# Kernel optimization log

Measured on AMD Instinct MI355X. Metric: run time of the kernel, lower is better.

Reference implementation:

```python
import jax, jax.numpy as jnp
import numpy as np

BN_EPS = 1e-5

def setup_inputs() -> dict:
    key = jax.random.key(0)
    ks = jax.random.split(key, 10)
    N, D, E, EL, L = 100000, 128, 1600000, 500000, 3
    return {
        "x": jax.random.normal(ks[0], (N, D), jnp.float32),
        "lin_w": jax.random.normal(ks[1], (D, D), jnp.float32) * 0.05,
        "lin_b": jax.random.normal(ks[2], (D,), jnp.float32) * 0.05,
        "W1": jax.random.normal(ks[3], (L, D, D), jnp.float32) * 0.05,
        "b1": jax.random.normal(ks[4], (L, D), jnp.float32) * 0.05,
        "gamma": jnp.ones((L, D), jnp.float32),
        "beta": jnp.zeros((L, D), jnp.float32),
        "W2": jax.random.normal(ks[5], (L, D, D), jnp.float32) * 0.05,
        "b2": jax.random.normal(ks[6], (L, D), jnp.float32) * 0.05,
        "edge_index": jax.random.randint(ks[7], (2, E), 0, N, jnp.int64),
        "edge_label_index": jax.random.randint(ks[8], (2, EL), 0, N, jnp.int64),
    }

def reference(x, lin_w, lin_b, W1, b1, gamma, beta, W2, b2, edge_index, edge_label_index):
    N = x.shape[0]
    src, dst = edge_index[0], edge_index[1]
    # node_lin: Linear(num_features -> hidden)
    h = x @ lin_w + lin_b  # [N, D]
    # 3 GINConv layers: out_i = MLP((1+eps)*h_i + sum_{j->i} h_j), eps = 0
    for l in range(3):
        agg = jax.ops.segment_sum(h[src], dst, num_segments=N)  # scatter-add over edges
        z = h + agg
        z = z @ W1[l] + b1[l]
        # BatchNorm1d in training mode: batch (per-node-dim) statistics, biased var
        mu = jnp.mean(z, axis=0)
        var = jnp.var(z, axis=0)
        z = (z - mu) * jax.lax.rsqrt(var + BN_EPS) * gamma[l] + beta[l]
        z = jax.nn.relu(z)
        z = z @ W2[l] + b2[l]
        h = jax.nn.relu(z)
    # Classifier: dot product of endpoint embeddings
    pred = jnp.sum(h[edge_label_index[0]] * h[edge_label_index[1]], axis=-1)  # [E_label]
    return pred
```

## Files before the change

kernel.cpp:

```cpp
#include <hip/hip_runtime.h>
#include <hip/hip_bf16.h>


typedef __attribute__((ext_vector_type(8))) short short8v;
typedef __attribute__((ext_vector_type(4))) float float4v;

#define NBLK_SORT 512

__device__ __forceinline__ unsigned short f2bf(float f) {
    union { float f; unsigned u; } v; v.f = f;
    unsigned u = v.u;
    unsigned r = u + 0x7fffu + ((u >> 16) & 1u);
    return (unsigned short)(r >> 16);
}
__device__ __forceinline__ float bf2f(unsigned short h) {
    union { unsigned u; float f; } v; v.u = ((unsigned)h) << 16;
    return v.f;
}
__device__ __forceinline__ float bfu_lo(unsigned u) {
    union { unsigned v; float f; } x; x.v = u << 16; return x.f;
}
__device__ __forceinline__ float bfu_hi(unsigned u) {
    union { unsigned v; float f; } x; x.v = u & 0xffff0000u; return x.f;
}
__device__ __forceinline__ unsigned pkbf(float x, float y) {
    __hip_bfloat162 t = __float22bfloat162_rn(float2{x, y});
    union { __hip_bfloat162 b; unsigned u; } c; c.b = t;
    return c.u;
}

__global__ __launch_bounds__(256) void prep_w(
    const float* __restrict__ lin_w, const float* __restrict__ W1,
    const float* __restrict__ W2,
    unsigned short* __restrict__ wt_hi, unsigned short* __restrict__ wt_lo)
{
    int idx = blockIdx.x * 256 + threadIdx.x;
    if (idx >= 7 * 16384) return;
    int m = idx >> 14;
    int r = idx & 16383;
    int k = r >> 7, n = r & 127;
    const float* src = (m == 0) ? lin_w
                     : (m <= 3) ? W1 + (size_t)(m - 1) * 16384
                                : W2 + (size_t)(m - 4) * 16384;
    float w = src[r];
    unsigned short hi = f2bf(w);
    unsigned short lo = f2bf(w - bf2f(hi));
    wt_hi[(size_t)m * 16384 + n * 128 + k] = hi;
    wt_lo[(size_t)m * 16384 + n * 128 + k] = lo;
}

__global__ __launch_bounds__(256) void chunk_count(
    const int* __restrict__ dst, int* __restrict__ cnt, int E, int nbc)
{
    __shared__ int l[1024];
    const int tid = threadIdx.x, b = blockIdx.x;
    for (int i = tid; i < nbc; i += 256) l[i] = 0;
    __syncthreads();
    const int per = (E + gridDim.x - 1) / gridDim.x;
    const int e0 = b * per, e1 = min(E, e0 + per);
    for (int e = e0 + tid; e < e1; e += 256)
        atomicAdd(&l[dst[e] >> 10], 1);
    __syncthreads();
    for (int c = tid; c < nbc; c += 256) cnt[c * gridDim.x + b] = l[c];
}

__global__ __launch_bounds__(256) void chunk_scan(
    int* __restrict__ cnt, int* __restrict__ chunkBase, int nbc)
{
    __shared__ int ctot[1024];
    __shared__ int cbase[1025];
    const int t = threadIdx.x;
    for (int c = t; c < nbc; c += 256) {
        int base = 0;
        for (int b = 0; b < NBLK_SORT; b++) {
            int x = cnt[c * NBLK_SORT + b];
            cnt[c * NBLK_SORT + b] = base;
            base += x;
        }
        ctot[c] = base;
    }
    __syncthreads();
    if (t == 0) {
        int acc = 0;
        for (int c = 0; c < nbc; c++) { cbase[c] = acc; acc += ctot[c]; }
        cbase[nbc] = acc;
    }
    __syncthreads();
    for (int c = t; c < nbc; c += 256) {
        const int cb = cbase[c];
        for (int b = 0; b < NBLK_SORT; b++) cnt[c * NBLK_SORT + b] += cb;
        chunkBase[c] = cb;
    }
    if (t == 0) chunkBase[nbc] = cbase[nbc];
}

__global__ __launch_bounds__(256) void bucket_scatter(
    const int* __restrict__ src, const int* __restrict__ dst,
    const int* __restrict__ cnt, int* __restrict__ temp, int E, int nbc)
{
    __shared__ int lcur[1024];
    const int tid = threadIdx.x, b = blockIdx.x;
    for (int c = tid; c < nbc; c += 256) lcur[c] = cnt[c * gridDim.x + b];
    __syncthreads();
    const int per = (E + gridDim.x - 1) / gridDim.x;
    const int e0 = b * per, e1 = min(E, e0 + per);
    for (int e = e0 + tid; e < e1; e += 256) {
        const int d = dst[e];
        const int pos = atomicAdd(&lcur[d >> 10], 1);
        temp[pos] = ((d & 1023) << 22) | src[e];
    }
}

__global__ __launch_bounds__(256) void chunk_place(
    const int* __restrict__ temp, const int* __restrict__ chunkBase,
    int* __restrict__ col, int* __restrict__ deg, int* __restrict__ rowptr,
    int N)
{
    __shared__ int lcnt[1024];
    __shared__ int lcur[1024];
    __shared__ int sh[256];
    const int tid = threadIdx.x, c = blockIdx.x;
    const int s = chunkBase[c], e2 = chunkBase[c + 1];

    for (int i = tid; i < 1024; i += 256) lcnt[i] = 0;
    __syncthreads();
    for (int i = s + tid; i < e2; i += 256)
        atomicAdd(&lcnt[((unsigned)temp[i]) >> 22], 1);
    __syncthreads();

    const int b4 = tid * 4;
    const int v0 = lcnt[b4], v1 = lcnt[b4 + 1], v2 = lcnt[b4 + 2], v3 = lcnt[b4 + 3];
    const int ts = v0 + v1 + v2 + v3;
    sh[tid] = ts;
    __syncthreads();
    for (int off = 1; off < 256; off <<= 1) {
        int x = (tid >= off) ? sh[tid - off] : 0;
        __syncthreads();
        sh[tid] += x;
        __syncthreads();
    }
    const int run = sh[tid] - ts;
    lcur[b4]     = s + run;
    lcur[b4 + 1] = s + run + v0;
    lcur[b4 + 2] = s + run + v0 + v1;
    lcur[b4 + 3] = s + run + v0 + v1 + v2;
    const int node0 = c << 10;
    if (node0 + b4 < N)     { deg[node0 + b4]     = v0; rowptr[node0 + b4]     = lcur[b4]; }
    if (node0 + b4 + 1 < N) { deg[node0 + b4 + 1] = v1; rowptr[node0 + b4 + 1] = lcur[b4 + 1]; }
    if (node0 + b4 + 2 < N) { deg[node0 + b4 + 2] = v2; rowptr[node0 + b4 + 2] = lcur[b4 + 2]; }
    if (node0 + b4 + 3 < N) { deg[node0 + b4 + 3] = v3; rowptr[node0 + b4 + 3] = lcur[b4 + 3]; }
    __syncthreads();

    for (int i = s + tid; i < e2; i += 256) {
        const unsigned p = (unsigned)temp[i];
        const int pos = atomicAdd(&lcur[p >> 22], 1);
        col[pos] = (int)(p & 0x3FFFFFu);
    }
}

__global__ __launch_bounds__(256) void gemm_mfma(
    const float* __restrict__ Ain32, const unsigned short* __restrict__ AinB,
    const int* __restrict__ rowptr, const int* __restrict__ deg,
    const int* __restrict__ col,
    const unsigned short* __restrict__ Wh, const unsigned short* __restrict__ Wl,
    const float* __restrict__ bias, const float* __restrict__ ss,
    unsigned short* __restrict__ outb, float* __restrict__ part,
    int N, int flags)
{
    __shared__ __align__(16) unsigned short As[64][136];
    const int tid = threadIdx.x;
    const int row0 = blockIdx.x * 64;

    if (flags & 32) {
        const int g = tid >> 4;
        const int l = tid & 15;
        #pragma unroll
        for (int rr = 0; rr < 4; rr++) {
            const int r = g + rr * 16;
            const int row = row0 + r;
            float4 a0 = make_float4(0.f, 0.f, 0.f, 0.f);
            float4 a1 = make_float4(0.f, 0.f, 0.f, 0.f);
            if (row < N) {
                const uint4 su = *(const uint4*)(AinB + (size_t)row * 128 + l * 8);
                a0.x = bfu_lo(su.x); a0.y = bfu_hi(su.x);
                a0.z = bfu_lo(su.y); a0.w = bfu_hi(su.y);
                a1.x = bfu_lo(su.z); a1.y = bfu_hi(su.z);
                a1.z = bfu_lo(su.w); a1.w = bfu_hi(su.w);
                const int start = rowptr[row];
                const int cnt = deg[row];
                int j = 0;
                for (; j + 1 < cnt; j += 2) {
                    const int c0i = col[start + j];
                    const int c1i = col[start + j + 1];
                    const uint4 u0 = *(const uint4*)(AinB + (size_t)c0i * 128 + l * 8);
                    const uint4 u1 = *(const uint4*)(AinB + (size_t)c1i * 128 + l * 8);
                    a0.x += bfu_lo(u0.x); a0.y += bfu_hi(u0.x);
                    a0.z += bfu_lo(u0.y); a0.w += bfu_hi(u0.y);
                    a1.x += bfu_lo(u0.z); a1.y += bfu_hi(u0.z);
                    a1.z += bfu_lo(u0.w); a1.w += bfu_hi(u0.w);
                    a0.x += bfu_lo(u1.x); a0.y += bfu_hi(u1.x);
                    a0.z += bfu_lo(u1.y); a0.w += bfu_hi(u1.y);
                    a1.x += bfu_lo(u1.z); a1.y += bfu_hi(u1.z);
                    a1.z += bfu_lo(u1.w); a1.w += bfu_hi(u1.w);
                }
                if (j < cnt) {
                    const int c0i = col[start + j];
                    const uint4 u0 = *(const uint4*)(AinB + (size_t)c0i * 128 + l * 8);
                    a0.x += bfu_lo(u0.x); a0.y += bfu_hi(u0.x);
                    a0.z += bfu_lo(u0.y); a0.w += bfu_hi(u0.y);
                    a1.x += bfu_lo(u0.z); a1.y += bfu_hi(u0.z);
                    a1.z += bfu_lo(u0.w); a1.w += bfu_hi(u0.w);
                }
            }
            uint4 uh;
            uh.x = pkbf(a0.x, a0.y);
            uh.y = pkbf(a0.z, a0.w);
            uh.z = pkbf(a1.x, a1.y);
            uh.w = pkbf(a1.z, a1.w);
            *(uint4*)&As[r][l * 8] = uh;
        }
    } else if (flags & 64) {
        for (int i = tid; i < 64 * 16; i += 256) {
            const int r = i >> 4, c8 = i & 15;
            const int row = row0 + r;
            if (row < N) {
                uint4 u = *(const uint4*)(AinB + (size_t)row * 128 + c8 * 8);
                if (flags & 1) {
                    float4 v0, v1;
                    v0.x = bfu_lo(u.x); v0.y = bfu_hi(u.x);
                    v0.z = bfu_lo(u.y); v0.w = bfu_hi(u.y);
                    v1.x = bfu_lo(u.z); v1.y = bfu_hi(u.z);
                    v1.z = bfu_lo(u.w); v1.w = bfu_hi(u.w);
                    const float4 sc0 = ((const float4*)ss)[c8 * 2];
                    const float4 sc1 = ((const float4*)ss)[c8 * 2 + 1];
                    const float4 sh0 = ((const float4*)(ss + 128))[c8 * 2];
                    const float4 sh1 = ((const float4*)(ss + 128))[c8 * 2 + 1];
                    v0.x = fmaxf(v0.x * sc0.x + sh0.x, 0.f);
                    v0.y = fmaxf(v0.y * sc0.y + sh0.y, 0.f);
                    v0.z = fmaxf(v0.z * sc0.z + sh0.z, 0.f);
                    v0.w = fmaxf(v0.w * sc0.w + sh0.w, 0.f);
                    v1.x = fmaxf(v1.x * sc1.x + sh1.x, 0.f);
                    v1.y = fmaxf(v1.y * sc1.y + sh1.y, 0.f);
                    v1.z = fmaxf(v1.z * sc1.z + sh1.z, 0.f);
                    v1.w = fmaxf(v1.w * sc1.w + sh1.w, 0.f);
                    u.x = pkbf(v0.x, v0.y);
                    u.y = pkbf(v0.z, v0.w);
                    u.z = pkbf(v1.x, v1.y);
                    u.w = pkbf(v1.z, v1.w);
                }
                *(uint4*)&As[r][c8 * 8] = u;
            } else {
                *(uint4*)&As[r][c8 * 8] = make_uint4(0, 0, 0, 0);
            }
        }
    } else {
        for (int i = tid; i < 64 * 32; i += 256) {
            const int r = i >> 5, c4 = i & 31;
            const int row = row0 + r;
            float4 v = make_float4(0.f, 0.f, 0.f, 0.f);
            if (row < N) v = ((const float4*)(Ain32 + (size_t)row * 128))[c4];
            uint2 uh;
            uh.x = pkbf(v.x, v.y);
            uh.y = pkbf(v.z, v.w);
            *(uint2*)&As[r][c4 * 4] = uh;
        }
    }
    __syncthreads();

    const int w    = tid >> 6;
    const int lane = tid & 63;
    const int ln   = lane & 15;
    const int lq   = lane >> 4;
    const int c0   = w * 32;

    float4v acc[4][2];
    #pragma unroll
    for (int nt = 0; nt < 2; nt++) {
        const float bv = bias[c0 + nt * 16 + ln];
        #pragma unroll
        for (int mt = 0; mt < 4; mt++) acc[mt][nt] = (float4v){bv, bv, bv, bv};
    }

    #pragma unroll
    for (int kc = 0; kc < 4; kc++) {
        const size_t b0 = (size_t)(c0 + ln) * 128 + kc * 32 + lq * 8;
        const size_t b1 = (size_t)(c0 + 16 + ln) * 128 + kc * 32 + lq * 8;
        const short8v bh0 = *(const short8v*)&Wh[b0];
        const short8v bl0 = *(const short8v*)&Wl[b0];
        const short8v bh1 = *(const short8v*)&Wh[b1];
        const short8v bl1 = *(const short8v*)&Wl[b1];
        #pragma unroll
        for (int mt = 0; mt < 4; mt++) {
            const short8v ah = *(const short8v*)&As[mt * 16 + ln][kc * 32 + lq * 8];
            acc[mt][0] = __builtin_amdgcn_mfma_f32_16x16x32_bf16(ah, bh0, acc[mt][0], 0, 0, 0);
            acc[mt][0] = __builtin_amdgcn_mfma_f32_16x16x32_bf16(ah, bl0, acc[mt][0], 0, 0, 0);
            acc[mt][1] = __builtin_amdgcn_mfma_f32_16x16x32_bf16(ah, bh1, acc[mt][1], 0, 0, 0);
            acc[mt][1] = __builtin_amdgcn_mfma_f32_16x16x32_bf16(ah, bl1, acc[mt][1], 0, 0, 0);
        }
    }

    #pragma unroll
    for (int mt = 0; mt < 4; mt++) {
        #pragma unroll
        for (int nt = 0; nt < 2; nt++) {
            const int colv = c0 + nt * 16 + ln;
            #pragma unroll
            for (int i = 0; i < 4; i++) {
                const int row = row0 + mt * 16 + lq * 4 + i;
                if (row < N) {
                    float v = acc[mt][nt][i];
                    if (flags & 2) v = fmaxf(v, 0.f);
                    outb[(size_t)row * 128 + colv] = f2bf(v);
                }
            }
        }
    }

    if (flags & 4) {
        #pragma unroll
        for (int nt = 0; nt < 2; nt++) {
            float s = 0.f, q = 0.f;
            #pragma unroll
            for (int mt = 0; mt < 4; mt++) {
                #pragma unroll
                for (int i = 0; i < 4; i++) {
                    const int row = row0 + mt * 16 + lq * 4 + i;
                    if (row < N) { const float v = acc[mt][nt][i]; s += v; q += v * v; }
                }
            }
            s += __shfl_xor(s, 16); s += __shfl_xor(s, 32);
            q += __shfl_xor(q, 16); q += __shfl_xor(q, 32);
            if (lq == 0) {
                const int colv = c0 + nt * 16 + ln;
                part[(size_t)colv * gridDim.x + blockIdx.x] = s;
                part[(size_t)(128 + colv) * gridDim.x + blockIdx.x] = q;
            }
        }
    }
}

__global__ __launch_bounds__(256) void bn_finalize(
    const float* __restrict__ part, int nblk, float invN,
    const float* __restrict__ gamma, const float* __restrict__ beta,
    float* __restrict__ ss)
{
    __shared__ float shs[256], shq[256];
    const int c = blockIdx.x, t = threadIdx.x;
    float s = 0.f, q = 0.f;
    for (int b = t; b < nblk; b += 256) {
        s += part[(size_t)c * nblk + b];
        q += part[(size_t)(128 + c) * nblk + b];
    }
    shs[t] = s; shq[t] = q;
    __syncthreads();
    for (int o = 128; o > 0; o >>= 1) {
        if (t < o) { shs[t] += shs[t + o]; shq[t] += shq[t + o]; }
        __syncthreads();
    }
    if (t == 0) {
        const float mu = shs[0] * invN;
        const float var = shq[0] * invN - mu * mu;
        const float sc = rsqrtf(fmaxf(var, 0.f) + 1e-5f) * gamma[c];
        ss[c] = sc;
        ss[128 + c] = beta[c] - mu * sc;
    }
}

__global__ __launch_bounds__(256) void edge_dot(
    const unsigned short* __restrict__ hb, const int* __restrict__ ia,
    const int* __restrict__ ib, float* __restrict__ out, int EL)
{
    const int stride = gridDim.x * blockDim.x;
    const long long total = (long long)EL * 16;
    for (long long i = (long long)blockIdx.x * blockDim.x + threadIdx.x; i < total; i += stride) {
        const int e = (int)(i >> 4);
        const int l = (int)(i & 15);
        const int a = ia[e];
        const int b = ib[e];
        const uint4 u = *(const uint4*)(hb + (size_t)a * 128 + l * 8);
        const uint4 v = *(const uint4*)(hb + (size_t)b * 128 + l * 8);
        float d = bfu_lo(u.x) * bfu_lo(v.x) + bfu_hi(u.x) * bfu_hi(v.x)
                + bfu_lo(u.y) * bfu_lo(v.y) + bfu_hi(u.y) * bfu_hi(v.y)
                + bfu_lo(u.z) * bfu_lo(v.z) + bfu_hi(u.z) * bfu_hi(v.z)
                + bfu_lo(u.w) * bfu_lo(v.w) + bfu_hi(u.w) * bfu_hi(v.w);
        d += __shfl_xor(d, 1); d += __shfl_xor(d, 2);
        d += __shfl_xor(d, 4); d += __shfl_xor(d, 8);
        if (l == 0) out[e] = d;
    }
}

extern "C" void kernel_launch(void* const* d_in, const int* in_sizes, int n_in,
                              void* d_out, int out_size, void* d_ws, size_t ws_size,
                              hipStream_t stream)
{
    const float* x     = (const float*)d_in[0];
    const float* lin_w = (const float*)d_in[1];
    const float* lin_b = (const float*)d_in[2];
    const float* W1    = (const float*)d_in[3];
    const float* b1    = (const float*)d_in[4];
    const float* gamma = (const float*)d_in[5];
    const float* beta  = (const float*)d_in[6];
    const float* W2    = (const float*)d_in[7];
    const float* b2    = (const float*)d_in[8];
    const int*   ei    = (const int*)d_in[9];
    const int*   eli   = (const int*)d_in[10];
    float* out = (float*)d_out;

    const int N  = in_sizes[0] / 128;
    const int E  = in_sizes[9] / 2;
    const int EL = in_sizes[10] / 2;
    const size_t nd = (size_t)N * 128;
    const int nbc = (N + 1023) >> 10;
    const int gemm_grid = (N + 63) / 64;

    unsigned short* hbH = (unsigned short*)d_ws;
    unsigned short* hbZ = hbH + nd;
    int*   deg    = (int*)(hbZ + nd);
    int*   rowptr = deg + N;
    int*   cnt    = rowptr + N;
    int*   chunkBase = cnt + (size_t)nbc * NBLK_SORT;
    int*   temp   = chunkBase + nbc + 1;
    int*   col    = temp + E;
    unsigned short* wt_hi = (unsigned short*)(col + E);
    unsigned short* wt_lo = wt_hi + 7 * 16384;
    float* part   = (float*)(wt_lo + 7 * 16384);
    float* ss     = part + (size_t)256 * gemm_grid;

    const float invN = 1.0f / (float)N;

    prep_w<<<448, 256, 0, stream>>>(lin_w, W1, W2, wt_hi, wt_lo);
    chunk_count<<<NBLK_SORT, 256, 0, stream>>>(ei + E, cnt, E, nbc);
    chunk_scan<<<1, 256, 0, stream>>>(cnt, chunkBase, nbc);
    bucket_scatter<<<NBLK_SORT, 256, 0, stream>>>(ei, ei + E, cnt, temp, E, nbc);
    chunk_place<<<nbc, 256, 0, stream>>>(temp, chunkBase, col, deg, rowptr, N);

    gemm_mfma<<<gemm_grid, 256, 0, stream>>>(x, nullptr, nullptr, nullptr, nullptr,
                                             wt_hi, wt_lo, lin_b, ss, hbH, part, N, 0);

    for (int l = 0; l < 3; l++) {
        const unsigned short* w1h = wt_hi + (size_t)(1 + l) * 16384;
        const unsigned short* w1l = wt_lo + (size_t)(1 + l) * 16384;
        const unsigned short* w2h = wt_hi + (size_t)(4 + l) * 16384;
        const unsigned short* w2l = wt_lo + (size_t)(4 + l) * 16384;
        gemm_mfma<<<gemm_grid, 256, 0, stream>>>(nullptr, hbH, rowptr, deg, col,
                                                 w1h, w1l, b1 + (size_t)l * 128,
                                                 ss, hbZ, part, N, 4 | 32 | 64);
        bn_finalize<<<128, 256, 0, stream>>>(part, gemm_grid, invN,
                                             gamma + (size_t)l * 128,
                                             beta + (size_t)l * 128, ss);
        gemm_mfma<<<gemm_grid, 256, 0, stream>>>(nullptr, hbZ, nullptr, nullptr, nullptr,
                                                 w2h, w2l, b2 + (size_t)l * 128,
                                                 ss, hbH, part, N, 1 | 2 | 64);
    }

    edge_dot<<<8192, 256, 0, stream>>>(hbH, eli, eli + EL, out, EL);
}
```

Before: 627.8 us.

## Parallelize chunk scan, split gather GEMM, enlarge stream GEMM tile

The single-block serial chunk_scan is replaced by a per-chunk parallel block scan (512 threads) plus a tiny kernel that scans chunk totals, with the chunk base added later in bucket_scatter. The GEMM kernel is split into a gather variant, whose neighbor loop is unrolled by four for more memory-level parallelism, and a streaming variant that handles 128 rows per block. The aim is to remove the serial scan bottleneck and to improve latency hiding and weight reuse. The larger tile raises register and LDS use per block, which may lower occupancy.

```diff
diff --git a/kernel.cpp b/kernel.cpp
--- a/kernel.cpp
+++ b/kernel.cpp
@@ -64,43 +64,43 @@
     for (int c = tid; c < nbc; c += 256) cnt[c * gridDim.x + b] = l[c];
 }
 
-__global__ __launch_bounds__(256) void chunk_scan(
-    int* __restrict__ cnt, int* __restrict__ chunkBase, int nbc)
-{
-    __shared__ int ctot[1024];
-    __shared__ int cbase[1025];
-    const int t = threadIdx.x;
-    for (int c = t; c < nbc; c += 256) {
-        int base = 0;
-        for (int b = 0; b < NBLK_SORT; b++) {
-            int x = cnt[c * NBLK_SORT + b];
-            cnt[c * NBLK_SORT + b] = base;
-            base += x;
-        }
-        ctot[c] = base;
-    }
-    __syncthreads();
-    if (t == 0) {
+__global__ __launch_bounds__(512) void scan_blocks(
+    int* __restrict__ cnt, int* __restrict__ ctot)
+{
+    __shared__ int sh[512];
+    const int c = blockIdx.x, t = threadIdx.x;
+    const int v = cnt[c * NBLK_SORT + t];
+    sh[t] = v;
+    __syncthreads();
+    for (int off = 1; off < 512; off <<= 1) {
+        int x = (t >= off) ? sh[t - off] : 0;
+        __syncthreads();
+        sh[t] += x;
+        __syncthreads();
+    }
+    cnt[c * NBLK_SORT + t] = sh[t] - v;
+    if (t == 511) ctot[c] = sh[511];
+}
+
+__global__ void scan_ctot(const int* __restrict__ ctot,
+                          int* __restrict__ chunkBase, int nbc)
+{
+    if (threadIdx.x == 0 && blockIdx.x == 0) {
         int acc = 0;
-        for (int c = 0; c < nbc; c++) { cbase[c] = acc; acc += ctot[c]; }
-        cbase[nbc] = acc;
-    }
-    __syncthreads();
-    for (int c = t; c < nbc; c += 256) {
-        const int cb = cbase[c];
-        for (int b = 0; b < NBLK_SORT; b++) cnt[c * NBLK_SORT + b] += cb;
-        chunkBase[c] = cb;
-    }
-    if (t == 0) chunkBase[nbc] = cbase[nbc];
+        for (int c = 0; c < nbc; c++) { chunkBase[c] = acc; acc += ctot[c]; }
+        chunkBase[nbc] = acc;
+    }
 }
 
 __global__ __launch_bounds__(256) void bucket_scatter(
     const int* __restrict__ src, const int* __restrict__ dst,
-    const int* __restrict__ cnt, int* __restrict__ temp, int E, int nbc)
+    const int* __restrict__ cnt, const int* __restrict__ chunkBase,
+    int* __restrict__ temp, int E, int nbc)
 {
     __shared__ int lcur[1024];
     const int tid = threadIdx.x, b = blockIdx.x;
-    for (int c = tid; c < nbc; c += 256) lcur[c] = cnt[c * gridDim.x + b];
+    for (int c = tid; c < nbc; c += 256)
+        lcur[c] = cnt[c * gridDim.x + b] + chunkBase[c];
     __syncthreads();
     const int per = (E + gridDim.x - 1) / gridDim.x;
     const int e0 = b * per, e1 = min(E, e0 + per);
@@ -158,73 +158,163 @@
     }
 }
 
-__global__ __launch_bounds__(256) void gemm_mfma(
-    const float* __restrict__ Ain32, const unsigned short* __restrict__ AinB,
+__global__ __launch_bounds__(256) void gemm_gather(
+    const unsigned short* __restrict__ AinB,
     const int* __restrict__ rowptr, const int* __restrict__ deg,
     const int* __restrict__ col,
     const unsigned short* __restrict__ Wh, const unsigned short* __restrict__ Wl,
-    const float* __restrict__ bias, const float* __restrict__ ss,
-    unsigned short* __restrict__ outb, float* __restrict__ part,
-    int N, int flags)
+    const float* __restrict__ bias,
+    unsigned short* __restrict__ outb, float* __restrict__ part, int N)
 {
     __shared__ __align__(16) unsigned short As[64][136];
     const int tid = threadIdx.x;
     const int row0 = blockIdx.x * 64;
 
-    if (flags & 32) {
-        const int g = tid >> 4;
-        const int l = tid & 15;
-        #pragma unroll
-        for (int rr = 0; rr < 4; rr++) {
-            const int r = g + rr * 16;
-            const int row = row0 + r;
-            float4 a0 = make_float4(0.f, 0.f, 0.f, 0.f);
-            float4 a1 = make_float4(0.f, 0.f, 0.f, 0.f);
-            if (row < N) {
-                const uint4 su = *(const uint4*)(AinB + (size_t)row * 128 + l * 8);
-                a0.x = bfu_lo(su.x); a0.y = bfu_hi(su.x);
-                a0.z = bfu_lo(su.y); a0.w = bfu_hi(su.y);
-                a1.x = bfu_lo(su.z); a1.y = bfu_hi(su.z);
-                a1.z = bfu_lo(su.w); a1.w = bfu_hi(su.w);
-                const int start = rowptr[row];
-                const int cnt = deg[row];
-                int j = 0;
-                for (; j + 1 < cnt; j += 2) {
-                    const int c0i = col[start + j];
-                    const int c1i = col[start + j + 1];
-                    const uint4 u0 = *(const uint4*)(AinB + (size_t)c0i * 128 + l * 8);
-                    const uint4 u1 = *(const uint4*)(AinB + (size_t)c1i * 128 + l * 8);
-                    a0.x += bfu_lo(u0.x); a0.y += bfu_hi(u0.x);
-                    a0.z += bfu_lo(u0.y); a0.w += bfu_hi(u0.y);
-                    a1.x += bfu_lo(u0.z); a1.y += bfu_hi(u0.z);
-                    a1.z += bfu_lo(u0.w); a1.w += bfu_hi(u0.w);
-                    a0.x += bfu_lo(u1.x); a0.y += bfu_hi(u1.x);
-                    a0.z += bfu_lo(u1.y); a0.w += bfu_hi(u1.y);
-                    a1.x += bfu_lo(u1.z); a1.y += bfu_hi(u1.z);
-                    a1.z += bfu_lo(u1.w); a1.w += bfu_hi(u1.w);
-                }
-                if (j < cnt) {
-                    const int c0i = col[start + j];
-                    const uint4 u0 = *(const uint4*)(AinB + (size_t)c0i * 128 + l * 8);
-                    a0.x += bfu_lo(u0.x); a0.y += bfu_hi(u0.x);
-                    a0.z += bfu_lo(u0.y); a0.w += bfu_hi(u0.y);
-                    a1.x += bfu_lo(u0.z); a1.y += bfu_hi(u0.z);
-                    a1.z += bfu_lo(u0.w); a1.w += bfu_hi(u0.w);
-                }
+    const int g = tid >> 4;
+    const int l = tid & 15;
+    #pragma unroll
+    for (int rr = 0; rr < 4; rr++) {
+        const int r = g + rr * 16;
+        const int row = row0 + r;
+        float4 a0 = make_float4(0.f, 0.f, 0.f, 0.f);
+        float4 a1 = make_float4(0.f, 0.f, 0.f, 0.f);
+        if (row < N) {
+            const uint4 su = *(const uint4*)(AinB + (size_t)row * 128 + l * 8);
+            a0.x = bfu_lo(su.x); a0.y = bfu_hi(su.x);
+            a0.z = bfu_lo(su.y); a0.w = bfu_hi(su.y);
+            a1.x = bfu_lo(su.z); a1.y = bfu_hi(su.z);
+            a1.z = bfu_lo(su.w); a1.w = bfu_hi(su.w);
+            const int start = rowptr[row];
+            const int cnt = deg[row];
+            int j = 0;
+            for (; j + 3 < cnt; j += 4) {
+                const int c0i = col[start + j];
+                const int c1i = col[start + j + 1];
+                const int c2i = col[start + j + 2];
+                const int c3i = col[start + j + 3];
+                const uint4 u0 = *(const uint4*)(AinB + (size_t)c0i * 128 + l * 8);
+                const uint4 u1 = *(const uint4*)(AinB + (size_t)c1i * 128 + l * 8);
+                const uint4 u2 = *(const uint4*)(AinB + (size_t)c2i * 128 + l * 8);
+                const uint4 u3 = *(const uint4*)(AinB + (size_t)c3i * 128 + l * 8);
+                a0.x += bfu_lo(u0.x); a0.y += bfu_hi(u0.x);
+                a0.z += bfu_lo(u0.y); a0.w += bfu_hi(u0.y);
+                a1.x += bfu_lo(u0.z); a1.y += bfu_hi(u0.z);
+                a1.z += bfu_lo(u0.w); a1.w += bfu_hi(u0.w);
+                a0.x += bfu_lo(u1.x); a0.y += bfu_hi(u1.x);
+                a0.z += bfu_lo(u1.y); a0.w += bfu_hi(u1.y);
+                a1.x += bfu_lo(u1.z); a1.y += bfu_hi(u1.z);
+                a1.z += bfu_lo(u1.w); a1.w += bfu_hi(u1.w);
+                a0.x += bfu_lo(u2.x); a0.y += bfu_hi(u2.x);
+                a0.z += bfu_lo(u2.y); a0.w += bfu_hi(u2.y);
+                a1.x += bfu_lo(u2.z); a1.y += bfu_hi(u2.z);
+                a1.z += bfu_lo(u2.w); a1.w += bfu_hi(u2.w);
+                a0.x += bfu_lo(u3.x); a0.y += bfu_hi(u3.x);
+                a0.z += bfu_lo(u3.y); a0.w += bfu_hi(u3.y);
+                a1.x += bfu_lo(u3.z); a1.y += bfu_hi(u3.z);
+                a1.z += bfu_lo(u3.w); a1.w += bfu_hi(u3.w);
             }
-            uint4 uh;
-            uh.x = pkbf(a0.x, a0.y);
-            uh.y = pkbf(a0.z, a0.w);
-            uh.z = pkbf(a1.x, a1.y);
-            uh.w = pkbf(a1.z, a1.w);
-            *(uint4*)&As[r][l * 8] = uh;
-        }
-    } else if (flags & 64) {
-        for (int i = tid; i < 64 * 16; i += 256) {
+            for (; j < cnt; j++) {
+                const int c0i = col[start + j];
+                const uint4 u0 = *(const uint4*)(AinB + (size_t)c0i * 128 + l * 8);
+                a0.x += bfu_lo(u0.x); a0.y += bfu_hi(u0.x);
+                a0.z += bfu_lo(u0.y); a0.w += bfu_hi(u0.y);
+                a1.x += bfu_lo(u0.z); a1.y += bfu_hi(u0.z);
+                a1.z += bfu_lo(u0.w); a1.w += bfu_hi(u0.w);
+            }
+        }
+        uint4 uh;
+        uh.x = pkbf(a0.x, a0.y);
+        uh.y = pkbf(a0.z, a0.w);
+        uh.z = pkbf(a1.x, a1.y);
+        uh.w = pkbf(a1.z, a1.w);
+        *(uint4*)&As[r][l * 8] = uh;
+    }
+    __syncthreads();
+
+    const int w    = tid >> 6;
+    const int lane = tid & 63;
+    const int ln   = lane & 15;
+    const int lq   = lane >> 4;
+    const int c0   = w * 32;
+
+    float4v acc[4][2];
+    #pragma unroll
+    for (int nt = 0; nt < 2; nt++) {
+        const float bv = bias[c0 + nt * 16 + ln];
+        #pragma unroll
+        for (int mt = 0; mt < 4; mt++) acc[mt][nt] = (float4v){bv, bv, bv, bv};
+    }
+
+    #pragma unroll
+    for (int kc = 0; kc < 4; kc++) {
+        const size_t b0 = (size_t)(c0 + ln) * 128 + kc * 32 + lq * 8;
+        const size_t b1 = (size_t)(c0 + 16 + ln) * 128 + kc * 32 + lq * 8;
+        const short8v bh0 = *(const short8v*)&Wh[b0];
+        const short8v bl0 = *(const short8v*)&Wl[b0];
+        const short8v bh1 = *(const short8v*)&Wh[b1];
+        const short8v bl1 = *(const short8v*)&Wl[b1];
+        #pragma unroll
+        for (int mt = 0; mt < 4; mt++) {
+            const short8v ah = *(const short8v*)&As[mt * 16 + ln][kc * 32 + lq * 8];
+            acc[mt][0] = __builtin_amdgcn_mfma_f32_16x16x32_bf16(ah, bh0, acc[mt][0], 0, 0, 0);
+            acc[mt][0] = __builtin_amdgcn_mfma_f32_16x16x32_bf16(ah, bl0, acc[mt][0], 0, 0, 0);
+            acc[mt][1] = __builtin_amdgcn_mfma_f32_16x16x32_bf16(ah, bh1, acc[mt][1], 0, 0, 0);
+            acc[mt][1] = __builtin_amdgcn_mfma_f32_16x16x32_bf16(ah, bl1, acc[mt][1], 0, 0, 0);
+        }
+    }
+
+    #pragma unroll
+    for (int mt = 0; mt < 4; mt++) {
+        #pragma unroll
+        for (int nt = 0; nt < 2; nt++) {
+            const int colv = c0 + nt * 16 + ln;
+            #pragma unroll
+            for (int i = 0; i < 4; i++) {
+                const int row = row0 + mt * 16 + lq * 4 + i;
+                if (row < N)
+                    outb[(size_t)row * 128 + colv] = f2bf(acc[mt][nt][i]);
+            }
+        }
+    }
+
+    #pragma unroll
+    for (int nt = 0; nt < 2; nt++) {
+        float s = 0.f, q = 0.f;
+        #pragma unroll
+        for (int mt = 0; mt < 4; mt++) {
+            #pragma unroll
+            for (int i = 0; i < 4; i++) {
+                const int row = row0 + mt * 16 + lq * 4 + i;
+                if (row < N) { const float v = acc[mt][nt][i]; s += v; q += v * v; }
+            }
+        }
+        s += __shfl_xor(s, 16); s += __shfl_xor(s, 32);
+        q += __shfl_xor(q, 16); q += __shfl_xor(q, 32);
+        if (lq == 0) {
+            const int colv = c0 + nt * 16 + ln;
+            part[(size_t)colv * gridDim.x + blockIdx.x] = s;
+            part[(size_t)(128 + colv) * gridDim.x + blockIdx.x] = q;
+        }
+    }
+}
+
+__global__ __launch_bounds__(256) void gemm_stream(
+    const float* __restrict__ Ain32, const unsigned short* __restrict__ AinB,
+    const unsigned short* __restrict__ Wh, const unsigned short* __restrict__ Wl,
+    const float* __restrict__ bias, const float* __restrict__ ss,
+    unsigned short* __restrict__ outb, int N, int flags)
+{
+    __shared__ __align__(16) unsigned short As[128][136];
+    const int tid = threadIdx.x;
+    const int row0 = blockIdx.x * 128;
+
+    if (flags & 64) {
+        for (int i = tid; i < 128 * 16; i += 256) {
             const int r = i >> 4, c8 = i & 15;
             const int row = row0 + r;
+            uint4 u = make_uint4(0, 0, 0, 0);
             if (row < N) {
-                uint4 u = *(const uint4*)(AinB + (size_t)row * 128 + c8 * 8);
+                u = *(const uint4*)(AinB + (size_t)row * 128 + c8 * 8);
                 if (flags & 1) {
                     float4 v0, v1;
                     v0.x = bfu_lo(u.x); v0.y = bfu_hi(u.x);
@@ -248,13 +338,11 @@
                     u.z = pkbf(v1.x, v1.y);
                     u.w = pkbf(v1.z, v1.w);
                 }
-                *(uint4*)&As[r][c8 * 8] = u;
-            } else {
-                *(uint4*)&As[r][c8 * 8] = make_uint4(0, 0, 0, 0);
             }
+            *(uint4*)&As[r][c8 * 8] = u;
         }
     } else {
-        for (int i = tid; i < 64 * 32; i += 256) {
+        for (int i = tid; i < 128 * 32; i += 256) {
             const int r = i >> 5, c4 = i & 31;
             const int row = row0 + r;
             float4 v = make_float4(0.f, 0.f, 0.f, 0.f);
@@ -273,12 +361,12 @@
     const int lq   = lane >> 4;
     const int c0   = w * 32;
 
-    float4v acc[4][2];
+    float4v acc[8][2];
     #pragma unroll
     for (int nt = 0; nt < 2; nt++) {
         const float bv = bias[c0 + nt * 16 + ln];
         #pragma unroll
-        for (int mt = 0; mt < 4; mt++) acc[mt][nt] = (float4v){bv, bv, bv, bv};
+        for (int mt = 0; mt < 8; mt++) acc[mt][nt] = (float4v){bv, bv, bv, bv};
     }
 
     #pragma unroll
@@ -290,7 +378,7 @@
         const short8v bh1 = *(const short8v*)&Wh[b1];
         const short8v bl1 = *(const short8v*)&Wl[b1];
         #pragma unroll
-        for (int mt = 0; mt < 4; mt++) {
+        for (int mt = 0; mt < 8; mt++) {
             const short8v ah = *(const short8v*)&As[mt * 16 + ln][kc * 32 + lq * 8];
             acc[mt][0] = __builtin_amdgcn_mfma_f32_16x16x32_bf16(ah, bh0, acc[mt][0], 0, 0, 0);
             acc[mt][0] = __builtin_amdgcn_mfma_f32_16x16x32_bf16(ah, bl0, acc[mt][0], 0, 0, 0);
@@ -300,7 +388,7 @@
     }
 
     #pragma unroll
-    for (int mt = 0; mt < 4; mt++) {
+    for (int mt = 0; mt < 8; mt++) {
         #pragma unroll
         for (int nt = 0; nt < 2; nt++) {
             const int colv = c0 + nt * 16 + ln;
@@ -312,28 +400,6 @@
                     if (flags & 2) v = fmaxf(v, 0.f);
                     outb[(size_t)row * 128 + colv] = f2bf(v);
                 }
-            }
-        }
-    }
-
-    if (flags & 4) {
-        #pragma unroll
-        for (int nt = 0; nt < 2; nt++) {
-            float s = 0.f, q = 0.f;
-            #pragma unroll
-            for (int mt = 0; mt < 4; mt++) {
-                #pragma unroll
-                for (int i = 0; i < 4; i++) {
-                    const int row = row0 + mt * 16 + lq * 4 + i;
-                    if (row < N) { const float v = acc[mt][nt][i]; s += v; q += v * v; }
-                }
-            }
-            s += __shfl_xor(s, 16); s += __shfl_xor(s, 32);
-            q += __shfl_xor(q, 16); q += __shfl_xor(q, 32);
-            if (lq == 0) {
-                const int colv = c0 + nt * 16 + ln;
-                part[(size_t)colv * gridDim.x + blockIdx.x] = s;
-                part[(size_t)(128 + colv) * gridDim.x + blockIdx.x] = q;
             }
         }
     }
@@ -411,46 +477,49 @@
     const int EL = in_sizes[10] / 2;
     const size_t nd = (size_t)N * 128;
     const int nbc = (N + 1023) >> 10;
-    const int gemm_grid = (N + 63) / 64;
+    const int g_grid = (N + 63) / 64;
+    const int s_grid = (N + 127) / 128;
 
     unsigned short* hbH = (unsigned short*)d_ws;
     unsigned short* hbZ = hbH + nd;
     int*   deg    = (int*)(hbZ + nd);
     int*   rowptr = deg + N;
     int*   cnt    = rowptr + N;
-    int*   chunkBase = cnt + (size_t)nbc * NBLK_SORT;
+    int*   ctot   = cnt + (size_t)nbc * NBLK_SORT;
+    int*   chunkBase = ctot + nbc;
     int*   temp   = chunkBase + nbc + 1;
     int*   col    = temp + E;
     unsigned short* wt_hi = (unsigned short*)(col + E);
     unsigned short* wt_lo = wt_hi + 7 * 16384;
     float* part   = (float*)(wt_lo + 7 * 16384);
-    float* ss     = part + (size_t)256 * gemm_grid;
+    float* ss     = part + (size_t)256 * g_grid;
 
     const float invN = 1.0f / (float)N;
 
     prep_w<<<448, 256, 0, stream>>>(lin_w, W1, W2, wt_hi, wt_lo);
     chunk_count<<<NBLK_SORT, 256, 0, stream>>>(ei + E, cnt, E, nbc);
-    chunk_scan<<<1, 256, 0, stream>>>(cnt, chunkBase, nbc);
-    bucket_scatter<<<NBLK_SORT, 256, 0, stream>>>(ei, ei + E, cnt, temp, E, nbc);
+    scan_blocks<<<nbc, 512, 0, stream>>>(cnt, ctot);
+    scan_ctot<<<1, 64, 0, stream>>>(ctot, chunkBase, nbc);
+    bucket_scatter<<<NBLK_SORT, 256, 0, stream>>>(ei, ei + E, cnt, chunkBase, temp, E, nbc);
     chunk_place<<<nbc, 256, 0, stream>>>(temp, chunkBase, col, deg, rowptr, N);
 
-    gemm_mfma<<<gemm_grid, 256, 0, stream>>>(x, nullptr, nullptr, nullptr, nullptr,
-                                             wt_hi, wt_lo, lin_b, ss, hbH, part, N, 0);
+    gemm_stream<<<s_grid, 256, 0, stream>>>(x, nullptr, wt_hi, wt_lo, lin_b, ss,
+                                            hbH, N, 0);
 
     for (int l = 0; l < 3; l++) {
         const unsigned short* w1h = wt_hi + (size_t)(1 + l) * 16384;
         const unsigned short* w1l = wt_lo + (size_t)(1 + l) * 16384;
         const unsigned short* w2h = wt_hi + (size_t)(4 + l) * 16384;
         const unsigned short* w2l = wt_lo + (size_t)(4 + l) * 16384;
-        gemm_mfma<<<gemm_grid, 256, 0, stream>>>(nullptr, hbH, rowptr, deg, col,
-                                                 w1h, w1l, b1 + (size_t)l * 128,
-                                                 ss, hbZ, part, N, 4 | 32 | 64);
-        bn_finalize<<<128, 256, 0, stream>>>(part, gemm_grid, invN,
+        gemm_gather<<<g_grid, 256, 0, stream>>>(hbH, rowptr, deg, col,
+                                                w1h, w1l, b1 + (size_t)l * 128,
+                                                hbZ, part, N);
+        bn_finalize<<<128, 256, 0, stream>>>(part, g_grid, invN,
                                              gamma + (size_t)l * 128,
                                              beta + (size_t)l * 128, ss);
-        gemm_mfma<<<gemm_grid, 256, 0, stream>>>(nullptr, hbZ, nullptr, nullptr, nullptr,
-                                                 w2h, w2l, b2 + (size_t)l * 128,
-                                                 ss, hbH, part, N, 1 | 2 | 64);
+        gemm_stream<<<s_grid, 256, 0, stream>>>(nullptr, hbZ, w2h, w2l,
+                                                b2 + (size_t)l * 128, ss,
+                                                hbH, N, 1 | 2 | 64);
     }
 
     edge_dot<<<8192, 256, 0, stream>>>(hbH, eli, eli + EL, out, EL);
```

New measurement: 550.3 us. -12.4%, faster.
